# Kernel optimization log

Measured on AMD Instinct MI355X. Metric: run time of the kernel, lower is better.

The kernel has to match this reference:

```python
import jax, jax.numpy as jnp
import numpy as np

H = 8      # num_heads
DH = 80    # head_dim = embed_dim // num_heads


def setup_inputs() -> dict:
    key = jax.random.key(0)
    ks = jax.random.split(key, 7)
    B, T, S = 8, 4096, 77
    hidden, embed, ctx = 640, 640, 768
    sc_h = 1.0 / np.sqrt(hidden)
    sc_c = 1.0 / np.sqrt(ctx)
    sc_e = 1.0 / np.sqrt(embed)
    return {
        "tokens": jax.random.normal(ks[0], (B, T, hidden), jnp.float32),
        "context": jax.random.normal(ks[1], (B, S, ctx), jnp.float32),
        "Wq": jax.random.normal(ks[2], (hidden, embed), jnp.float32) * sc_h,
        "Wk": jax.random.normal(ks[3], (ctx, embed), jnp.float32) * sc_c,
        "Wv": jax.random.normal(ks[4], (ctx, embed), jnp.float32) * sc_c,
        "Wo": jax.random.normal(ks[5], (embed, hidden), jnp.float32) * sc_e,
        "bo": jnp.zeros((hidden,), jnp.float32),
    }


def reference(tokens, context, Wq, Wk, Wv, Wo, bo):
    B, T, _ = tokens.shape
    S = context.shape[1]
    Q = (tokens @ Wq).reshape(B, T, H, DH)    # B T H D
    K = (context @ Wk).reshape(B, S, H, DH)   # B S H D
    V = (context @ Wv).reshape(B, S, H, DH)
    scores = jnp.einsum('bthd,bshd->bhts', Q, K) / jnp.sqrt(jnp.float32(DH))
    attn = jax.nn.softmax(scores, axis=-1)    # B H T S
    ctx_vecs = jnp.einsum('bhts,bshd->bthd', attn, V).reshape(B, T, H * DH)
    return ctx_vecs @ Wo + bo
```

## Files before the change

kernel.cpp:

```cpp
#include <hip/hip_runtime.h>
#include <hip/hip_bf16.h>
#include <hip/hip_fp16.h>

typedef __attribute__((ext_vector_type(4))) float f32x4;
typedef __attribute__((ext_vector_type(8))) _Float16 f16x8;
typedef __attribute__((ext_vector_type(8))) unsigned short u16x8;

__device__ __forceinline__ unsigned short f2h(float f) {
    _Float16 h = (_Float16)f;
    return __builtin_bit_cast(unsigned short, h);
}

#define GLOAD_LDS16(gp, lp) __builtin_amdgcn_global_load_lds( \
    (const __attribute__((address_space(1))) void*)(gp), \
    (__attribute__((address_space(3))) void*)(lp), 16, 0, 0)
#define PRIO1() __builtin_amdgcn_s_setprio(1)
#define PRIO0() __builtin_amdgcn_s_setprio(0)

__global__ void cvt_kernel(const float* __restrict__ in, ushort* __restrict__ out, int n4) {
    int stride = gridDim.x * blockDim.x;
    for (int i = blockIdx.x * blockDim.x + threadIdx.x; i < n4; i += stride) {
        float4 v = ((const float4*)in)[i];
        ushort4 o;
        o.x = f2h(v.x); o.y = f2h(v.y); o.z = f2h(v.z); o.w = f2h(v.w);
        ((ushort4*)out)[i] = o;
    }
}

__global__ void transpose_cvt2(const float* __restrict__ Wk, const float* __restrict__ Wv,
                               ushort* __restrict__ WkvT) {
    __shared__ float tile[32][33];
    const int z = blockIdx.z;
    const float* src = z ? Wv : Wk;
    ushort* dst = WkvT + (size_t)z * 640 * 768;
    const int R = 768, C = 640;
    int tx = threadIdx.x, ty = threadIdx.y;
    int c = blockIdx.x * 32 + tx;
    int r0 = blockIdx.y * 32;
#pragma unroll
    for (int i = ty; i < 32; i += 8) {
        int r = r0 + i;
        tile[i][tx] = (r < R && c < C) ? src[(size_t)r * C + c] : 0.f;
    }
    __syncthreads();
    int rr = r0 + tx;
    int c0 = blockIdx.x * 32;
#pragma unroll
    for (int i = ty; i < 32; i += 8) {
        int cc = c0 + i;
        if (cc < C && rr < R) dst[(size_t)cc * R + rr] = f2h(tile[tx][i]);
    }
}

__global__ void pack_wfrag(const float* __restrict__ W, ushort* __restrict__ WF) {
    int g = blockIdx.x * 256 + threadIdx.x;
    if (g >= 51200) return;
    int lane = g & 63;
    int fi = (g >> 6) % 10;
    int kt = ((g >> 6) / 10) % 10;
    int h  = (g >> 6) / 100;
    int ni = fi >> 1, kk = fi & 1;
    int n  = h * 80 + ni * 16 + (lane & 15);
    int k0 = kt * 64 + kk * 32 + (lane >> 4) * 8;
    u16x8 o;
#pragma unroll
    for (int e = 0; e < 8; ++e) o[e] = f2h(W[(size_t)(k0 + e) * 640 + n]);
    *(u16x8*)&WF[(size_t)g * 8] = o;
}

__global__ void pack_kvfrag(const ushort* __restrict__ KVb,
                            ushort* __restrict__ KF, ushort* __restrict__ VF) {
    int g = blockIdx.x * 256 + threadIdx.x;
    if (g >= 61440) return;
    int lane = g & 63;
    int fi = (g >> 6) % 15;
    int bh = (g >> 6) / 15;
    int b = bh >> 3, h = bh & 7;
    int ni = fi / 3, kk = fi % 3;
    int l15 = lane & 15, lhi = lane >> 4;
    int sr = ni * 16 + l15; if (sr > 76) sr = 76;
    int d0 = kk * 32 + lhi * 8;
    u16x8 ko, vo;
#pragma unroll
    for (int e = 0; e < 8; ++e)
        ko[e] = KVb[((size_t)b * 77 + sr) * 1280 + h * 80 + d0 + e];
    int dv = ni * 16 + l15;
    int s0 = kk * 32 + lhi * 8;
#pragma unroll
    for (int e = 0; e < 8; ++e) {
        int s = s0 + e;
        vo[e] = (s < 77) ? KVb[((size_t)b * 77 + s) * 1280 + 640 + h * 80 + dv] : (ushort)0;
    }
    *(u16x8*)&KF[(size_t)g * 8] = ko;
    *(u16x8*)&VF[(size_t)g * 8] = vo;
}

template<int OUT_F16, int HAS_BIAS>
__global__ __launch_bounds__(256) void gemm_bt(
    const ushort* __restrict__ A, const ushort* __restrict__ Bt,
    void* __restrict__ C, const float* __restrict__ bias,
    int M, int N, int K)
{
    __shared__ ushort As[128 * 64];
    __shared__ ushort Bs[128 * 64];
    const int tid = threadIdx.x;
    const int lane = tid & 63;
    const int w = tid >> 6;
    const int wr = (w >> 1) * 64, wc = (w & 1) * 64;
    const int m0 = blockIdx.x * 128, n0 = blockIdx.y * 128;
    const int l15 = lane & 15, lhi = lane >> 4;

    f32x4 acc[4][4] = {};

    for (int k0 = 0; k0 < K; k0 += 64) {
        __syncthreads();
#pragma unroll
        for (int i = 0; i < 4; ++i) {
            int c = i * 256 + tid;
            int m = m0 + (c >> 3);
            if (m > M - 1) m = M - 1;
            GLOAD_LDS16(A + (size_t)m * K + k0 + (c & 7) * 8, &As[c * 8]);
        }
#pragma unroll
        for (int i = 0; i < 4; ++i) {
            int c = i * 256 + tid;
            GLOAD_LDS16(Bt + (size_t)(n0 + (c >> 3)) * K + k0 + (c & 7) * 8, &Bs[c * 8]);
        }
        __syncthreads();
#pragma unroll
        for (int kk = 0; kk < 2; ++kk) {
            f16x8 af[4], bfr[4];
#pragma unroll
            for (int mi = 0; mi < 4; ++mi)
                af[mi] = *(const f16x8*)&As[(wr + mi * 16 + l15) * 64 + kk * 32 + lhi * 8];
#pragma unroll
            for (int ni = 0; ni < 4; ++ni)
                bfr[ni] = *(const f16x8*)&Bs[(wc + ni * 16 + l15) * 64 + kk * 32 + lhi * 8];
#pragma unroll
            for (int mi = 0; mi < 4; ++mi)
#pragma unroll
                for (int ni = 0; ni < 4; ++ni)
                    acc[mi][ni] = __builtin_amdgcn_mfma_f32_16x16x32_f16(
                        af[mi], bfr[ni], acc[mi][ni], 0, 0, 0);
        }
    }

#pragma unroll
    for (int mi = 0; mi < 4; ++mi)
#pragma unroll
        for (int ni = 0; ni < 4; ++ni)
#pragma unroll
            for (int r = 0; r < 4; ++r) {
                int row = m0 + wr + mi * 16 + lhi * 4 + r;
                int col = n0 + wc + ni * 16 + l15;
                if (row < M) {
                    float v = acc[mi][ni][r];
                    if (HAS_BIAS) v += bias[col];
                    if (OUT_F16) ((ushort*)C)[(size_t)row * N + col] = f2h(v);
                    else         ((float*)C)[(size_t)row * N + col] = v;
                }
            }
}

__global__ __launch_bounds__(512) void fused_attn(
    const float* __restrict__ tokens, const ushort* __restrict__ WqF,
    const ushort* __restrict__ KF, const ushort* __restrict__ VF,
    const ushort* __restrict__ WoF, const float* __restrict__ bo,
    float* __restrict__ out)
{
    __shared__ __align__(16) ushort lds[81920];
    const int tid = threadIdx.x;
    const int lane = tid & 63;
    const int w = tid >> 6;
    const int l15 = lane & 15, lhi = lane >> 4;
    const int tt = blockIdx.x, b = blockIdx.y;
    const size_t rowbase = (size_t)b * 4096 + (size_t)tt * 128;

    const ushort* WqFb = WqF + (size_t)w * 10 * 5120;
    const ushort* WoFb = WoF + (size_t)w * 10 * 5120;
    const ushort* KFb  = KF + (size_t)(b * 8 + w) * 15 * 512;
    const ushort* VFb  = VF + (size_t)(b * 8 + w) * 15 * 512;

    const int r0s = tid >> 3;
    const int r1s = r0s + 64;
    const int s0s = tid & 7;
    const int d0s = r0s * 64 + (s0s ^ (r0s & 7)) * 8;
    const int d1s = r1s * 64 + (s0s ^ (r1s & 7)) * 8;

#define STAGE_LOAD(C, A0, B0, A1, B1) do { \
    const float* p0_ = tokens + (rowbase + r0s) * 640 + (C) * 64 + s0s * 8; \
    const float* p1_ = tokens + (rowbase + r1s) * 640 + (C) * 64 + s0s * 8; \
    A0 = ((const float4*)p0_)[0]; B0 = ((const float4*)p0_)[1]; \
    A1 = ((const float4*)p1_)[0]; B1 = ((const float4*)p1_)[1]; \
} while (0)
#define STAGE_WRITE(BUF, A0, B0, A1, B1) do { \
    u16x8 o0_, o1_; \
    o0_[0]=f2h(A0.x); o0_[1]=f2h(A0.y); o0_[2]=f2h(A0.z); o0_[3]=f2h(A0.w); \
    o0_[4]=f2h(B0.x); o0_[5]=f2h(B0.y); o0_[6]=f2h(B0.z); o0_[7]=f2h(B0.w); \
    o1_[0]=f2h(A1.x); o1_[1]=f2h(A1.y); o1_[2]=f2h(A1.z); o1_[3]=f2h(A1.w); \
    o1_[4]=f2h(B1.x); o1_[5]=f2h(B1.y); o1_[6]=f2h(B1.z); o1_[7]=f2h(B1.w); \
    *(u16x8*)&lds[(BUF) * 8192 + d0s] = o0_; \
    *(u16x8*)&lds[(BUF) * 8192 + d1s] = o1_; \
} while (0)

    {
        float4 a0, b0, a1, b1, c0, d0, c1, d1;
        STAGE_LOAD(0, a0, b0, a1, b1);
        STAGE_LOAD(1, c0, d0, c1, d1);
        STAGE_WRITE(0, a0, b0, a1, b1);
        STAGE_WRITE(1, c0, d0, c1, d1);
    }
    f16x8 PE[5], PO[5];
#pragma unroll
    for (int f = 0; f < 5; ++f)
        PE[f] = *(const f16x8*)(WqFb + (f * 2) * 512 + lane * 8);
    __syncthreads();

    f32x4 acc[8][5];
#define ZACC() do { \
    _Pragma("unroll") for (int i_ = 0; i_ < 8; ++i_) \
    _Pragma("unroll") for (int j_ = 0; j_ < 5; ++j_) \
        acc[i_][j_] = (f32x4){0.f, 0.f, 0.f, 0.f}; \
} while (0)

#define MHALF(PC, PN, WB, CURB, RSTR, SBASE, KK, NKT, NKK, DOPF) do { \
    if (DOPF) { \
        _Pragma("unroll") for (int f = 0; f < 5; ++f) \
            (PN)[f] = *(const f16x8*)((WB) + (size_t)(NKT) * 5120 + (f * 2 + (NKK)) * 512 + lane * 8); \
    } \
    PRIO1(); \
    _Pragma("unroll") for (int mi = 0; mi < 8; ++mi) { \
        int row_ = mi * 16 + l15; \
        f16x8 a_ = *(const f16x8*)&lds[(CURB) + row_ * (RSTR) + ((SBASE) + (((KK) * 4 + lhi) ^ (row_ & 7))) * 8]; \
        _Pragma("unroll") for (int ni = 0; ni < 5; ++ni) \
            acc[mi][ni] = __builtin_amdgcn_mfma_f32_16x16x32_f16(a_, (PC)[ni], acc[mi][ni], 0, 0, 0); \
    } \
    PRIO0(); \
} while (0)

    ZACC();
    for (int kt = 0; kt < 10; ++kt) {
        const int curb = (kt & 1) * 8192;
        float4 a0, b0, a1, b1;
        if (kt < 8) STAGE_LOAD(kt + 2, a0, b0, a1, b1);
        MHALF(PE, PO, WqFb, curb, 64, 0, 0, kt, 1, 1);
        MHALF(PO, PE, WqFb, curb, 64, 0, 1, kt + 1, 0, kt < 9);
        __syncthreads();
        if (kt < 8) STAGE_WRITE(kt & 1, a0, b0, a1, b1);
    }

    const int qoff = w * 10240;
#pragma unroll
    for (int mi = 0; mi < 8; ++mi)
#pragma unroll
        for (int ni = 0; ni < 5; ++ni)
#pragma unroll
            for (int r = 0; r < 4; ++r)
                lds[qoff + (mi*16 + lhi*4 + r)*80 + ni*16 + l15] = f2h(acc[mi][ni][r]);
    __builtin_amdgcn_sched_barrier(0);

    const f16x8 zf = {};
#define ATT_KK(PC, PN, FB, KK, NKK, DOPF) do { \
    if (DOPF) { \
        _Pragma("unroll") for (int f = 0; f < 5; ++f) \
            (PN)[f] = *(const f16x8*)((FB) + (f * 3 + (NKK)) * 512 + lane * 8); \
    } \
    const int kcol = ((KK) < 2) ? ((KK)*32 + lhi*8) : (64 + (lhi & 1)*8); \
    PRIO1(); \
    _Pragma("unroll") for (int mi = 0; mi < 8; ++mi) { \
        f16x8 aq_ = *(const f16x8*)&lds[qoff + (mi*16 + l15)*80 + kcol]; \
        if ((KK) == 2 && lhi >= 2) aq_ = zf; \
        _Pragma("unroll") for (int ni = 0; ni < 5; ++ni) \
            acc[mi][ni] = __builtin_amdgcn_mfma_f32_16x16x32_f16(aq_, (PC)[ni], acc[mi][ni], 0, 0, 0); \
    } \
    PRIO0(); \
} while (0)

    ZACC();
#pragma unroll
    for (int f = 0; f < 5; ++f)
        PE[f] = *(const f16x8*)(KFb + (f * 3) * 512 + lane * 8);
    ATT_KK(PE, PO, KFb, 0, 1, 1);
    ATT_KK(PO, PE, KFb, 1, 2, 1);
    ATT_KK(PE, PO, KFb, 2, 0, 0);
    __builtin_amdgcn_sched_barrier(0);

    const float sc = 0.11180339887498949f;
#pragma unroll
    for (int mi = 0; mi < 8; ++mi)
#pragma unroll
        for (int r = 0; r < 4; ++r) {
            float v0 = acc[mi][0][r]*sc, v1 = acc[mi][1][r]*sc, v2 = acc[mi][2][r]*sc,
                  v3 = acc[mi][3][r]*sc, v4 = acc[mi][4][r]*sc;
            bool ok4 = l15 < 13;
            float mx = fmaxf(fmaxf(v0, v1), fmaxf(v2, v3));
            if (ok4) mx = fmaxf(mx, v4);
#pragma unroll
            for (int off = 1; off < 16; off <<= 1) mx = fmaxf(mx, __shfl_xor(mx, off, 16));
            float p0 = __expf(v0-mx), p1 = __expf(v1-mx), p2 = __expf(v2-mx), p3 = __expf(v3-mx);
            float p4 = ok4 ? __expf(v4-mx) : 0.f;
            float sm = p0+p1+p2+p3+p4;
#pragma unroll
            for (int off = 1; off < 16; off <<= 1) sm += __shfl_xor(sm, off, 16);
            float inv = 1.f / sm;
            int row = mi*16 + lhi*4 + r;
            lds[qoff + row*80 + 0*16 + l15] = f2h(p0*inv);
            lds[qoff + row*80 + 1*16 + l15] = f2h(p1*inv);
            lds[qoff + row*80 + 2*16 + l15] = f2h(p2*inv);
            lds[qoff + row*80 + 3*16 + l15] = f2h(p3*inv);
            lds[qoff + row*80 + 4*16 + l15] = f2h(p4*inv);
        }
    __builtin_amdgcn_sched_barrier(0);

    ZACC();
#pragma unroll
    for (int f = 0; f < 5; ++f)
        PE[f] = *(const f16x8*)(VFb + (f * 3) * 512 + lane * 8);
    ATT_KK(PE, PO, VFb, 0, 1, 1);
    ATT_KK(PO, PE, VFb, 1, 2, 1);
    ATT_KK(PE, PO, VFb, 2, 0, 0);
#undef ATT_KK
    __syncthreads();

#pragma unroll
    for (int mi = 0; mi < 8; ++mi)
#pragma unroll
        for (int ni = 0; ni < 5; ++ni)
#pragma unroll
            for (int r = 0; r < 4; ++r) {
                int row = mi*16 + lhi*4 + r;
                int col = w*80 + ni*16 + l15;
                int slot = col >> 3;
                int phys = (slot & ~7) | ((slot ^ row) & 7);
                lds[row*640 + phys*8 + (col & 7)] = f2h(acc[mi][ni][r]);
            }
    __syncthreads();

    ZACC();
#pragma unroll
    for (int f = 0; f < 5; ++f)
        PE[f] = *(const f16x8*)(WoFb + (f * 2) * 512 + lane * 8);
    for (int kt = 0; kt < 10; ++kt) {
        MHALF(PE, PO, WoFb, 0, 640, kt * 8, 0, kt, 1, 1);
        MHALF(PO, PE, WoFb, 0, 640, kt * 8, 1, kt + 1, 0, kt < 9);
    }
#undef MHALF
#undef ZACC

#pragma unroll
    for (int ni = 0; ni < 5; ++ni) {
        int col = w*80 + ni*16 + l15;
        float bvl = bo[col];
#pragma unroll
        for (int mi = 0; mi < 8; ++mi)
#pragma unroll
            for (int r = 0; r < 4; ++r)
                out[(rowbase + mi*16 + lhi*4 + r) * 640 + col] = acc[mi][ni][r] + bvl;
    }
#undef STAGE_LOAD
#undef STAGE_WRITE
}

extern "C" void kernel_launch(void* const* d_in, const int* in_sizes, int n_in,
                              void* d_out, int out_size, void* d_ws, size_t ws_size,
                              hipStream_t stream) {
    (void)in_sizes; (void)n_in; (void)out_size; (void)ws_size;
    const float* tokens  = (const float*)d_in[0];
    const float* context = (const float*)d_in[1];
    const float* Wq = (const float*)d_in[2];
    const float* Wk = (const float*)d_in[3];
    const float* Wv = (const float*)d_in[4];
    const float* Wo = (const float*)d_in[5];
    const float* bo = (const float*)d_in[6];
    float* out = (float*)d_out;

    ushort* ws   = (ushort*)d_ws;
    ushort* ctx16 = ws;
    ushort* WkvT = ctx16 + (size_t)616 * 768;
    ushort* KVb  = WkvT + (size_t)1280 * 768;
    ushort* WqF  = KVb  + (size_t)616 * 1280;
    ushort* WoF  = WqF  + (size_t)640 * 640;
    ushort* KF   = WoF  + (size_t)640 * 640;
    ushort* VF   = KF   + (size_t)61440 * 8;

    cvt_kernel<<<462, 256, 0, stream>>>(context, ctx16, 616 * 768 / 4);
    transpose_cvt2<<<dim3(20, 24, 2), dim3(32, 8), 0, stream>>>(Wk, Wv, WkvT);
    pack_wfrag<<<200, 256, 0, stream>>>(Wq, WqF);
    pack_wfrag<<<200, 256, 0, stream>>>(Wo, WoF);
    gemm_bt<1, 0><<<dim3(5, 10), 256, 0, stream>>>(ctx16, WkvT, KVb, nullptr, 616, 1280, 768);
    pack_kvfrag<<<240, 256, 0, stream>>>(KVb, KF, VF);
    fused_attn<<<dim3(32, 8), 512, 0, stream>>>(tokens, WqF, KF, VF, WoF, bo, out);
}
```

Measured before the change: 118.0 us.

## Split each attention block's rows across two wave groups with 1024-thread blocks

The fused attention kernel now uses 64-row tiles and 1024-thread blocks. Sixteen waves are arranged as 8 heads times 2 row halves, so each wave's accumulator shrinks from 8x5 to 2x5 MFMA tiles and the LDS footprint halves. The grid doubles to 512 blocks. The aim is to cut register pressure and raise waves per CU and parallelism. The trade-offs: each head's Wq, K, V and Wo fragments are now fetched by twice as many waves, and token staging drops from two chunks ahead to one.

```diff
diff --git a/kernel.cpp b/kernel.cpp
--- a/kernel.cpp
+++ b/kernel.cpp
@@ -162,53 +162,51 @@
             }
 }
 
-__global__ __launch_bounds__(512) void fused_attn(
+__global__ __launch_bounds__(1024, 1) void fused_attn(
     const float* __restrict__ tokens, const ushort* __restrict__ WqF,
     const ushort* __restrict__ KF, const ushort* __restrict__ VF,
     const ushort* __restrict__ WoF, const float* __restrict__ bo,
     float* __restrict__ out)
 {
-    __shared__ __align__(16) ushort lds[81920];
+    __shared__ __align__(16) ushort lds[40960];
     const int tid = threadIdx.x;
     const int lane = tid & 63;
     const int w = tid >> 6;
+    const int h = w & 7;
+    const int rh = w >> 3;
     const int l15 = lane & 15, lhi = lane >> 4;
     const int tt = blockIdx.x, b = blockIdx.y;
-    const size_t rowbase = (size_t)b * 4096 + (size_t)tt * 128;
-
-    const ushort* WqFb = WqF + (size_t)w * 10 * 5120;
-    const ushort* WoFb = WoF + (size_t)w * 10 * 5120;
-    const ushort* KFb  = KF + (size_t)(b * 8 + w) * 15 * 512;
-    const ushort* VFb  = VF + (size_t)(b * 8 + w) * 15 * 512;
-
-    const int r0s = tid >> 3;
-    const int r1s = r0s + 64;
-    const int s0s = tid & 7;
-    const int d0s = r0s * 64 + (s0s ^ (r0s & 7)) * 8;
-    const int d1s = r1s * 64 + (s0s ^ (r1s & 7)) * 8;
-
-#define STAGE_LOAD(C, A0, B0, A1, B1) do { \
-    const float* p0_ = tokens + (rowbase + r0s) * 640 + (C) * 64 + s0s * 8; \
-    const float* p1_ = tokens + (rowbase + r1s) * 640 + (C) * 64 + s0s * 8; \
-    A0 = ((const float4*)p0_)[0]; B0 = ((const float4*)p0_)[1]; \
-    A1 = ((const float4*)p1_)[0]; B1 = ((const float4*)p1_)[1]; \
-} while (0)
-#define STAGE_WRITE(BUF, A0, B0, A1, B1) do { \
-    u16x8 o0_, o1_; \
-    o0_[0]=f2h(A0.x); o0_[1]=f2h(A0.y); o0_[2]=f2h(A0.z); o0_[3]=f2h(A0.w); \
-    o0_[4]=f2h(B0.x); o0_[5]=f2h(B0.y); o0_[6]=f2h(B0.z); o0_[7]=f2h(B0.w); \
-    o1_[0]=f2h(A1.x); o1_[1]=f2h(A1.y); o1_[2]=f2h(A1.z); o1_[3]=f2h(A1.w); \
-    o1_[4]=f2h(B1.x); o1_[5]=f2h(B1.y); o1_[6]=f2h(B1.z); o1_[7]=f2h(B1.w); \
-    *(u16x8*)&lds[(BUF) * 8192 + d0s] = o0_; \
-    *(u16x8*)&lds[(BUF) * 8192 + d1s] = o1_; \
+    const size_t rowbase = (size_t)b * 4096 + (size_t)tt * 64;
+
+    const ushort* WqFb = WqF + (size_t)h * 10 * 5120;
+    const ushort* WoFb = WoF + (size_t)h * 10 * 5120;
+    const ushort* KFb  = KF + (size_t)(b * 8 + h) * 15 * 512;
+    const ushort* VFb  = VF + (size_t)(b * 8 + h) * 15 * 512;
+
+    const bool stager = tid < 512;
+    const int rs = (tid & 511) >> 3;
+    const int ss = tid & 7;
+    const int ds = rs * 64 + (ss ^ (rs & 7)) * 8;
+
+#define STAGE_LOAD(C, A0, B0) do { \
+    if (stager) { \
+        const float* p_ = tokens + (rowbase + rs) * 640 + (C) * 64 + ss * 8; \
+        A0 = ((const float4*)p_)[0]; B0 = ((const float4*)p_)[1]; \
+    } \
+} while (0)
+#define STAGE_WRITE(BUF, A0, B0) do { \
+    if (stager) { \
+        u16x8 o_; \
+        o_[0]=f2h(A0.x); o_[1]=f2h(A0.y); o_[2]=f2h(A0.z); o_[3]=f2h(A0.w); \
+        o_[4]=f2h(B0.x); o_[5]=f2h(B0.y); o_[6]=f2h(B0.z); o_[7]=f2h(B0.w); \
+        *(u16x8*)&lds[(BUF) * 4096 + ds] = o_; \
+    } \
 } while (0)
 
     {
-        float4 a0, b0, a1, b1, c0, d0, c1, d1;
-        STAGE_LOAD(0, a0, b0, a1, b1);
-        STAGE_LOAD(1, c0, d0, c1, d1);
-        STAGE_WRITE(0, a0, b0, a1, b1);
-        STAGE_WRITE(1, c0, d0, c1, d1);
+        float4 a0, b0;
+        STAGE_LOAD(0, a0, b0);
+        STAGE_WRITE(0, a0, b0);
     }
     f16x8 PE[5], PO[5];
 #pragma unroll
@@ -216,9 +214,9 @@
         PE[f] = *(const f16x8*)(WqFb + (f * 2) * 512 + lane * 8);
     __syncthreads();
 
-    f32x4 acc[8][5];
+    f32x4 acc[2][5];
 #define ZACC() do { \
-    _Pragma("unroll") for (int i_ = 0; i_ < 8; ++i_) \
+    _Pragma("unroll") for (int i_ = 0; i_ < 2; ++i_) \
     _Pragma("unroll") for (int j_ = 0; j_ < 5; ++j_) \
         acc[i_][j_] = (f32x4){0.f, 0.f, 0.f, 0.f}; \
 } while (0)
@@ -229,8 +227,8 @@
             (PN)[f] = *(const f16x8*)((WB) + (size_t)(NKT) * 5120 + (f * 2 + (NKK)) * 512 + lane * 8); \
     } \
     PRIO1(); \
-    _Pragma("unroll") for (int mi = 0; mi < 8; ++mi) { \
-        int row_ = mi * 16 + l15; \
+    _Pragma("unroll") for (int mi = 0; mi < 2; ++mi) { \
+        int row_ = rh * 32 + mi * 16 + l15; \
         f16x8 a_ = *(const f16x8*)&lds[(CURB) + row_ * (RSTR) + ((SBASE) + (((KK) * 4 + lhi) ^ (row_ & 7))) * 8]; \
         _Pragma("unroll") for (int ni = 0; ni < 5; ++ni) \
             acc[mi][ni] = __builtin_amdgcn_mfma_f32_16x16x32_f16(a_, (PC)[ni], acc[mi][ni], 0, 0, 0); \
@@ -240,18 +238,18 @@
 
     ZACC();
     for (int kt = 0; kt < 10; ++kt) {
-        const int curb = (kt & 1) * 8192;
-        float4 a0, b0, a1, b1;
-        if (kt < 8) STAGE_LOAD(kt + 2, a0, b0, a1, b1);
+        const int curb = (kt & 1) * 4096;
+        float4 a0, b0;
+        if (kt < 9) STAGE_LOAD(kt + 1, a0, b0);
         MHALF(PE, PO, WqFb, curb, 64, 0, 0, kt, 1, 1);
         MHALF(PO, PE, WqFb, curb, 64, 0, 1, kt + 1, 0, kt < 9);
+        if (kt < 9) STAGE_WRITE((kt + 1) & 1, a0, b0);
         __syncthreads();
-        if (kt < 8) STAGE_WRITE(kt & 1, a0, b0, a1, b1);
-    }
-
-    const int qoff = w * 10240;
-#pragma unroll
-    for (int mi = 0; mi < 8; ++mi)
+    }
+
+    const int qoff = w * 2560;
+#pragma unroll
+    for (int mi = 0; mi < 2; ++mi)
 #pragma unroll
         for (int ni = 0; ni < 5; ++ni)
 #pragma unroll
@@ -267,7 +265,7 @@
     } \
     const int kcol = ((KK) < 2) ? ((KK)*32 + lhi*8) : (64 + (lhi & 1)*8); \
     PRIO1(); \
-    _Pragma("unroll") for (int mi = 0; mi < 8; ++mi) { \
+    _Pragma("unroll") for (int mi = 0; mi < 2; ++mi) { \
         f16x8 aq_ = *(const f16x8*)&lds[qoff + (mi*16 + l15)*80 + kcol]; \
         if ((KK) == 2 && lhi >= 2) aq_ = zf; \
         _Pragma("unroll") for (int ni = 0; ni < 5; ++ni) \
@@ -287,7 +285,7 @@
 
     const float sc = 0.11180339887498949f;
 #pragma unroll
-    for (int mi = 0; mi < 8; ++mi)
+    for (int mi = 0; mi < 2; ++mi)
 #pragma unroll
         for (int r = 0; r < 4; ++r) {
             float v0 = acc[mi][0][r]*sc, v1 = acc[mi][1][r]*sc, v2 = acc[mi][2][r]*sc,
@@ -323,13 +321,13 @@
     __syncthreads();
 
 #pragma unroll
-    for (int mi = 0; mi < 8; ++mi)
+    for (int mi = 0; mi < 2; ++mi)
 #pragma unroll
         for (int ni = 0; ni < 5; ++ni)
 #pragma unroll
             for (int r = 0; r < 4; ++r) {
-                int row = mi*16 + lhi*4 + r;
-                int col = w*80 + ni*16 + l15;
+                int row = rh*32 + mi*16 + lhi*4 + r;
+                int col = h*80 + ni*16 + l15;
                 int slot = col >> 3;
                 int phys = (slot & ~7) | ((slot ^ row) & 7);
                 lds[row*640 + phys*8 + (col & 7)] = f2h(acc[mi][ni][r]);
@@ -349,13 +347,13 @@
 
 #pragma unroll
     for (int ni = 0; ni < 5; ++ni) {
-        int col = w*80 + ni*16 + l15;
+        int col = h*80 + ni*16 + l15;
         float bvl = bo[col];
 #pragma unroll
-        for (int mi = 0; mi < 8; ++mi)
+        for (int mi = 0; mi < 2; ++mi)
 #pragma unroll
             for (int r = 0; r < 4; ++r)
-                out[(rowbase + mi*16 + lhi*4 + r) * 640 + col] = acc[mi][ni][r] + bvl;
+                out[(rowbase + rh*32 + mi*16 + lhi*4 + r) * 640 + col] = acc[mi][ni][r] + bvl;
     }
 #undef STAGE_LOAD
 #undef STAGE_WRITE
@@ -389,5 +387,5 @@
     pack_wfrag<<<200, 256, 0, stream>>>(Wo, WoF);
     gemm_bt<1, 0><<<dim3(5, 10), 256, 0, stream>>>(ctx16, WkvT, KVb, nullptr, 616, 1280, 768);
     pack_kvfrag<<<240, 256, 0, stream>>>(KVb, KF, VF);
-    fused_attn<<<dim3(32, 8), 512, 0, stream>>>(tokens, WqF, KF, VF, WoF, bo, out);
-}
+    fused_attn<<<dim3(64, 8), 1024, 0, stream>>>(tokens, WqF, KF, VF, WoF, bo, out);
+}
```

Result: slower. 135.4 us (+14.7%).
